# Kernel optimization log

Hardware: AMD Instinct MI355X
Metric: run time of the kernel (lower is better)

The kernel has to match this reference:

```python
import jax, jax.numpy as jnp
import numpy as np

DIM = 256
HEADS = 8
HEAD_DIM = DIM // HEADS
B = 8
HH, WW = 32, 32
N = HH * WW
TABLE = (2 * HH - 1) * (2 * WW - 1)  # 3969
CPB_HID = 512


def _l2norm(t, eps=1e-12):
    # matches torch F.normalize(dim=-1): x / max(||x||, eps)
    n = jnp.sqrt(jnp.sum(t * t, axis=-1, keepdims=True))
    return t / jnp.maximum(n, eps)


def setup_inputs() -> dict:
    key = jax.random.key(0)
    ks = jax.random.split(key, 12)
    x = jax.random.normal(ks[0], (B, N, DIM), dtype=jnp.float32)
    relative_pos_index = jax.random.randint(ks[1], (N, N), 0, TABLE)
    relative_coords_table = jax.random.normal(ks[2], (TABLE, 2), dtype=jnp.float32)
    s = 0.02
    qkv_w = jax.random.normal(ks[3], (3 * DIM, DIM), dtype=jnp.float32) * s
    qkv_b = jnp.zeros((3 * DIM,), dtype=jnp.float32)
    query_embedding = jax.random.normal(ks[4], (HEADS, 1, HEAD_DIM), dtype=jnp.float32) * s
    # temperature init: log(exp(1/0.24) - 1) so softplus(temperature) = 1/0.24
    temperature = jnp.full((HEADS, 1, 1), float(np.log(np.expm1(1.0 / 0.24))), dtype=jnp.float32)
    proj_w = jax.random.normal(ks[5], (DIM, DIM), dtype=jnp.float32) * s
    proj_b = jnp.zeros((DIM,), dtype=jnp.float32)
    cpb_fc1_w = jax.random.normal(ks[6], (CPB_HID, 2), dtype=jnp.float32) * s
    cpb_fc1_b = jnp.zeros((CPB_HID,), dtype=jnp.float32)
    cpb_fc2_w = jax.random.normal(ks[7], (HEADS, CPB_HID), dtype=jnp.float32) * s
    cpb_fc2_b = jnp.zeros((HEADS,), dtype=jnp.float32)
    return dict(x=x, H=HH, W=WW, relative_pos_index=relative_pos_index,
                relative_coords_table=relative_coords_table,
                qkv_w=qkv_w, qkv_b=qkv_b, query_embedding=query_embedding,
                temperature=temperature, proj_w=proj_w, proj_b=proj_b,
                cpb_fc1_w=cpb_fc1_w, cpb_fc1_b=cpb_fc1_b,
                cpb_fc2_w=cpb_fc2_w, cpb_fc2_b=cpb_fc2_b)


def reference(x, H, W, relative_pos_index, relative_coords_table,
              qkv_w, qkv_b, query_embedding, temperature,
              proj_w, proj_b, cpb_fc1_w, cpb_fc1_b, cpb_fc2_w, cpb_fc2_b):
    Bc, Nc, C = x.shape
    seq_length_scale = jnp.asarray(np.log(HH * WW), dtype=x.dtype)  # from init input_resolution
    # qkv projection -> [B, heads, N, head_dim] each
    qkv = (x @ qkv_w.T + qkv_b).reshape(Bc, Nc, 3 * HEADS, HEAD_DIM).transpose(0, 2, 1, 3)
    q, k, v = qkv[:, :HEADS], qkv[:, HEADS:2 * HEADS], qkv[:, 2 * HEADS:]
    # CPB relative position bias: small MLP over coord table, then NxN gather
    h = jax.nn.relu(relative_coords_table @ cpb_fc1_w.T + cpb_fc1_b)  # [T, 512]
    table = (h @ cpb_fc2_w.T + cpb_fc2_b).T                           # [heads, T]
    rel_bias = table[:, relative_pos_index.reshape(-1)].reshape(HEADS, Nc, Nc)
    # cosine attention with learned temperature
    qn = _l2norm(q) + query_embedding[None]                           # [B, heads, N, hd]
    scale = jax.nn.softplus(temperature) * seq_length_scale           # [heads, 1, 1]
    attn = jnp.einsum('bhnd,bhmd->bhnm', qn * scale[None], _l2norm(k)) + rel_bias[None]
    attn = jax.nn.softmax(attn, axis=-1)
    out = jnp.einsum('bhnm,bhmd->bhnd', attn, v).transpose(0, 2, 1, 3).reshape(Bc, Nc, C)
    return out @ proj_w.T + proj_b
```

## Files before the change

kernel.cpp:

```cpp
#include <hip/hip_runtime.h>
#include <hip/hip_bf16.h>
#include <cstddef>
#include <cstdint>

typedef float v4f __attribute__((ext_vector_type(4)));
typedef short v8s __attribute__((ext_vector_type(8)));
typedef _Float16 v8h __attribute__((ext_vector_type(8)));

__device__ __forceinline__ uint32_t fbits(float x){ uint32_t u; __builtin_memcpy(&u,&x,4); return u; }
__device__ __forceinline__ float ffrom(uint32_t u){ float f; __builtin_memcpy(&f,&u,4); return f; }
__device__ __forceinline__ short bf_rh(float x){ return (short)((fbits(x)+0x8000u)>>16); }
__device__ __forceinline__ uint32_t pack_bf_rh(float a, float b){
    uint32_t ua = fbits(a)+0x8000u, ub = fbits(b)+0x8000u;
#if __has_builtin(__builtin_amdgcn_perm)
    return __builtin_amdgcn_perm(ub, ua, 0x07060302u);
#else
    return (ua>>16) | (ub & 0xFFFF0000u);
#endif
}
__device__ __forceinline__ short f2h(float x){ _Float16 h = (_Float16)x; short s; __builtin_memcpy(&s,&h,2); return s; }
#if __has_builtin(__builtin_amdgcn_exp2f)
#define EXP2(x) __builtin_amdgcn_exp2f(x)
#else
#define EXP2(x) exp2f(x)
#endif

__device__ __forceinline__ void gld16(const void* g, void* l) {
    __builtin_amdgcn_global_load_lds(
        (const __attribute__((address_space(1))) unsigned int*)g,
        (__attribute__((address_space(3))) unsigned int*)l, 16, 0, 0);
}
#define MFMA(a,b,c)  __builtin_amdgcn_mfma_f32_16x16x32_bf16((a),(b),(c),0,0,0)
#define MFMAH(a,b,c) __builtin_amdgcn_mfma_f32_16x16x32_f16((a),(b),(c),0,0,0)

#define LOG2E 1.4426950408889634f

__global__ __launch_bounds__(256)
void prep_kernel(const float* __restrict__ x,  short* __restrict__ xh,
                 const float* __restrict__ wq, short* __restrict__ wqh,
                 const float* __restrict__ wp, short* __restrict__ wph,
                 const float* __restrict__ rct,
                 const float* __restrict__ fc1w, const float* __restrict__ fc1b,
                 const float* __restrict__ fc2w, const float* __restrict__ fc2b,
                 float* __restrict__ table)
{
    __shared__ float s1[1024];
    __shared__ float sb[512];
    __shared__ float s2[4096];
    int bid = blockIdx.x;
    int tid = threadIdx.x;
    if (bid < 1152) {
        const float* src; short* dh; int base8;
        if (bid < 1024)      { src = x;  dh = xh;  base8 = bid * 256; }
        else if (bid < 1120) { src = wq; dh = wqh; base8 = (bid-1024) * 256; }
        else                 { src = wp; dh = wph; base8 = (bid-1120) * 256; }
        int e0 = (base8 + tid) * 8;
        int m  = e0 >> 8;
        int k  = e0 & 255;
        int kt = k >> 6, c = (k >> 3) & 7;
        float4 f0 = *(const float4*)(src + e0);
        float4 f1 = *(const float4*)(src + e0 + 4);
        float v[8] = {f0.x,f0.y,f0.z,f0.w,f1.x,f1.y,f1.z,f1.w};
        v8s hi;
        #pragma unroll
        for (int j = 0; j < 8; ++j) hi[j] = f2h(v[j]);
        int dst = m*256 + kt*64 + ((c ^ (m & 7)) << 3);
        *(v8s*)&dh[dst] = hi;
    } else {
        int cbid = bid - 1152;
        for (int i = tid; i < 1024; i += 256) s1[i] = fc1w[i];
        for (int i = tid; i < 512;  i += 256) sb[i] = fc1b[i];
        for (int i = tid; i < 4096; i += 256) s2[i] = fc2w[i];
        __syncthreads();
        int rl = tid >> 2, jp = tid & 3;
        bool ok = rl < 63;
        int r = cbid * 63 + rl;
        float c0 = ok ? rct[2*r]   : 0.f;
        float c1 = ok ? rct[2*r+1] : 0.f;
        float a[8] = {0,0,0,0,0,0,0,0};
        int j0 = jp * 128;
        #pragma unroll 4
        for (int j = j0; j < j0 + 128; ++j) {
            float hv = fmaxf(c0*s1[2*j] + c1*s1[2*j+1] + sb[j], 0.0f);
            #pragma unroll
            for (int hh = 0; hh < 8; ++hh) a[hh] += hv * s2[hh*512 + j];
        }
        #pragma unroll
        for (int hh = 0; hh < 8; ++hh) {
            a[hh] += __shfl_xor(a[hh], 1);
            a[hh] += __shfl_xor(a[hh], 2);
        }
        if (ok && jp == 0) {
            #pragma unroll
            for (int hh = 0; hh < 8; ++hh) table[hh*3969 + r] = a[hh] + fc2b[hh];
        }
    }
}

__global__ __launch_bounds__(256)
void qkv_bias_kernel(const short* __restrict__ xh, const short* __restrict__ wqh,
                     const float* __restrict__ qkvb,
                     short* __restrict__ qh, short* __restrict__ kh,
                     short* __restrict__ vt,
                     const float* __restrict__ qe, const float* __restrict__ temp,
                     const float* __restrict__ tblf, const int* __restrict__ rpi,
                     short* __restrict__ biasM)
{
    __shared__ __align__(16) char smem[49152];
    int bid  = blockIdx.x;
    int tid  = threadIdx.x;
    int w    = tid >> 6;
    int lane = tid & 63;
    int t    = lane & 15;
    int quad = lane >> 4;

    if (bid < 768) {
        short* A0 = (short*)smem;
        short* A1 = A0 + 128*64;
        short* W0 = A1 + 128*64;
        short* W1 = W0 + 64*64;
        int n0 = (bid % 12) * 64, m0 = (bid / 12) * 128;
        int Mw = (w >> 1) * 64, Nw = (w & 1) * 32;

        v4f acc[4][2];
        #pragma unroll
        for (int mt = 0; mt < 4; ++mt)
            #pragma unroll
            for (int nt = 0; nt < 2; ++nt) acc[mt][nt] = (v4f){0,0,0,0};

        int lr8 = lane >> 3, lc8 = lane & 7;
        #pragma unroll 1
        for (int kt2 = 0; kt2 < 2; ++kt2) {
            __syncthreads();
            #pragma unroll
            for (int half = 0; half < 2; ++half) {
                int kt = kt2*2 + half;
                short* Ad = half ? A1 : A0;
                short* Wd = half ? W1 : W0;
                #pragma unroll
                for (int i = 0; i < 4; ++i) {
                    size_t grow = (size_t)(m0 + w*32 + i*8 + lr8) * 256 + kt*64 + lc8*8;
                    gld16(xh + grow, Ad + (w*32 + i*8) * 64);
                }
                #pragma unroll
                for (int i = 0; i < 2; ++i) {
                    size_t grow = (size_t)(n0 + w*16 + i*8 + lr8) * 256 + kt*64 + lc8*8;
                    gld16(wqh + grow, Wd + (w*16 + i*8) * 64);
                }
            }
            __syncthreads();
            #pragma unroll
            for (int half = 0; half < 2; ++half) {
                const short* As = half ? A1 : A0;
                const short* Ws = half ? W1 : W0;
                #pragma unroll
                for (int kk = 0; kk < 2; ++kk) {
                    int cp = ((kk*4 + quad) ^ (t & 7)) << 3;
                    v8h bh8[2];
                    #pragma unroll
                    for (int nt = 0; nt < 2; ++nt)
                        bh8[nt] = *(const v8h*)&Ws[(Nw + nt*16 + t)*64 + cp];
                    #pragma unroll
                    for (int mt = 0; mt < 4; ++mt) {
                        v8h ah = *(const v8h*)&As[(Mw + mt*16 + t)*64 + cp];
                        #pragma unroll
                        for (int nt = 0; nt < 2; ++nt)
                            acc[mt][nt] = MFMAH(ah, bh8[nt], acc[mt][nt]);
                    }
                }
            }
        }

        #pragma unroll
        for (int nt = 0; nt < 2; ++nt) {
            float bv = qkvb[n0 + Nw + nt*16 + t];
            #pragma unroll
            for (int mt = 0; mt < 4; ++mt)
                #pragma unroll
                for (int r = 0; r < 4; ++r) acc[mt][nt][r] += bv;
        }

        int which = n0 >> 8;
        if (which < 2) {
            int head = ((n0 + Nw) >> 5) & 7;
            float scale = 0.f;
            if (which == 0)
                scale = log1pf(__expf(temp[head])) * 10.0f;
            #pragma unroll
            for (int mt = 0; mt < 4; ++mt)
                #pragma unroll
                for (int r = 0; r < 4; ++r) {
                    float a0 = acc[mt][0][r], a1 = acc[mt][1][r];
                    float s = a0*a0 + a1*a1;
                    s += __shfl_xor(s, 1); s += __shfl_xor(s, 2);
                    s += __shfl_xor(s, 4); s += __shfl_xor(s, 8);
                    float inv = 1.0f / fmaxf(sqrtf(s), 1e-12f);
                    int m = m0 + Mw + mt*16 + quad*4 + r;
                    int b = m >> 10, nrow = m & 1023;
                    if (which == 0) {
                        size_t rowoff = (((size_t)b*8 + head)*1024 + nrow) * 32;
                        #pragma unroll
                        for (int nt = 0; nt < 2; ++nt) {
                            int d = nt*16 + t;
                            float val = (acc[mt][nt][r] * inv + qe[head*32 + d]) * scale;
                            qh[rowoff + d] = f2h(val);
                        }
                    } else {
                        int kk = nrow & 63;
                        int p  = (kk & 3)*16 + (kk >> 2);
                        int prow = (nrow & ~63) | p;
                        int swk = (kk >> 3) & 3;
                        size_t rowoff = (((size_t)b*8 + head)*1024 + prow) * 32;
                        #pragma unroll
                        for (int nt = 0; nt < 2; ++nt) {
                            int d = nt*16 + t;
                            int dpos = (((d >> 3) ^ swk) << 3) | (d & 7);
                            kh[rowoff + dpos] = f2h(acc[mt][nt][r] * inv);
                        }
                    }
                }
        } else {
            __syncthreads();
            short* VT = (short*)smem;
            #pragma unroll
            for (int mt = 0; mt < 4; ++mt)
                #pragma unroll
                for (int nt = 0; nt < 2; ++nt) {
                    int cl = Nw + nt*16 + t;
                    #pragma unroll
                    for (int r = 0; r < 4; ++r) {
                        int rl = Mw + mt*16 + quad*4 + r;
                        VT[cl*136 + rl] = bf_rh(acc[mt][nt][r]);
                    }
                }
            __syncthreads();
            int b = m0 >> 10;
            int keybase = m0 & 1023;
            int headbase = ((n0 - 512) >> 5) & 7;
            int cl = tid >> 2;
            int dim = cl & 31;
            int hd  = headbase + (cl >> 5);
            size_t obase = (((size_t)b*8 + hd)*32 + dim) * 1024 + keybase;
            #pragma unroll
            for (int p = 0; p < 4; ++p) {
                int ci  = (tid & 3) * 4 + p;
                int ktl = ci >> 3, c = ci & 7;
                v8s val = *(const v8s*)&VT[cl*136 + ktl*64 + c*8];
                *(v8s*)&vt[obase + ktl*64 + ((c ^ (dim & 7)) << 3)] = val;
            }
        }
    } else {
        float* tb = (float*)smem;
        int b2  = bid - 768;
        int h   = b2 & 7;
        int q16 = b2 >> 3;
        for (int i = tid; i < 3969; i += 256) tb[i] = tblf[h*3969 + i] * LOG2E;
        __syncthreads();
        int row0 = q16*16 + quad*4;
        #pragma unroll 1
        for (int kk = 0; kk < 4; ++kk) {
            int kt = w*4 + kk;
            #pragma unroll
            for (int g = 0; g < 4; ++g) {
                float o[4];
                #pragma unroll
                for (int r = 0; r < 4; ++r)
                    o[r] = tb[rpi[(size_t)(row0 + r)*1024 + kt*64 + 4*t + g]];
                uint2 pk;
                pk.x = pack_bf_rh(o[0], o[1]);
                pk.y = pack_bf_rh(o[2], o[3]);
                size_t base = ((((size_t)(h*64 + q16)*16 + kt)*4 + g)*64 + lane)*4;
                *(uint2*)(biasM + base) = pk;
            }
        }
    }
}

__global__ __launch_bounds__(512)
void attn_mfma(const short* __restrict__ qh, const short* __restrict__ kh,
               const short* __restrict__ vt,  const short* __restrict__ biasM,
               short* __restrict__ yh)
{
    __shared__ __align__(16) short Kh_s[2][2048];
    __shared__ __align__(16) short Vt_s[2][2048];
    __shared__ __align__(16) short Ps[8][16][68];

    int bh  = blockIdx.x & 63;
    int qt  = blockIdx.x >> 6;
    int h   = bh & 7;
    int b   = bh >> 3;
    int tid = threadIdx.x;
    int w    = tid >> 6;
    int lane = tid & 63;
    int t    = lane & 15;
    int quad = lane >> 4;

    size_t qoff = ((size_t)bh*1024 + qt*128 + w*16 + t) * 32 + quad*8;
    v8h qf = *(const v8h*)(qh + qoff);

    v4f Oacc[2] = {{0,0,0,0},{0,0,0,0}};
    float lsum[4] = {0,0,0,0};

    size_t kgbase = (size_t)bh * 32768;
    const short* bmb = biasM + ((size_t)(h*64 + qt*8 + w) * 16) * 1024 + lane*4;
    int qrow0 = qt*128 + w*16 + quad*4;
    int swzS = (quad ^ ((t >> 1) & 3)) << 3;
    int lr8 = lane >> 3, lc8 = lane & 7;

    if (w < 4)
        gld16(kh + kgbase + w*512 + lane*8, &Kh_s[0][w*512]);
    else
        gld16(vt + kgbase + (size_t)((w-4)*8 + lr8)*1024 + lc8*8, &Vt_s[0][(w-4)*512]);
    uint2 curb[4];
    #pragma unroll
    for (int g = 0; g < 4; ++g) curb[g] = *(const uint2*)(bmb + g*256);

    #pragma unroll 1
    for (int kt = 0; kt < 16; ++kt) {
        int cur = kt & 1;
        __syncthreads();
        uint2 nxtb[4];
        if (kt < 15) {
            int nkt = kt + 1, nb = cur ^ 1;
            if (w < 4)
                gld16(kh + kgbase + (size_t)nkt*2048 + w*512 + lane*8, &Kh_s[nb][w*512]);
            else
                gld16(vt + kgbase + (size_t)((w-4)*8 + lr8)*1024 + nkt*64 + lc8*8,
                      &Vt_s[nb][(w-4)*512]);
            const short* bp = bmb + (size_t)nkt*1024;
            #pragma unroll
            for (int g = 0; g < 4; ++g) nxtb[g] = *(const uint2*)(bp + g*256);
        }

        v4f S[4];
        #pragma unroll
        for (int g = 0; g < 4; ++g) {
            v8h kb = *(const v8h*)&Kh_s[cur][(g*16 + t)*32 + swzS];
            v4f c;
            c[0] = ffrom(curb[g].x << 16);
            c[1] = ffrom(curb[g].x & 0xFFFF0000u);
            c[2] = ffrom(curb[g].y << 16);
            c[3] = ffrom(curb[g].y & 0xFFFF0000u);
            S[g] = MFMAH(qf, kb, c);
        }

        #pragma unroll
        for (int r = 0; r < 4; ++r) {
            float p0 = EXP2(S[0][r]);
            float p1 = EXP2(S[1][r]);
            float p2 = EXP2(S[2][r]);
            float p3 = EXP2(S[3][r]);
            lsum[r] += (p0 + p1) + (p2 + p3);
            uint2 pk;
            pk.x = pack_bf_rh(p0, p1);
            pk.y = pack_bf_rh(p2, p3);
            *(uint2*)&Ps[w][quad*4 + r][t*4] = pk;
        }

        #pragma unroll
        for (int ks = 0; ks < 2; ++ks) {
            v8s pf = *(const v8s*)&Ps[w][t][ks*32 + quad*8];
            int vsw = ((ks*4 + quad) ^ (t & 7)) << 3;
            #pragma unroll
            for (int g = 0; g < 2; ++g) {
                v8s vf = *(const v8s*)&Vt_s[cur][(g*16 + t)*64 + vsw];
                Oacc[g] = MFMA(pf, vf, Oacc[g]);
            }
        }
        #pragma unroll
        for (int g = 0; g < 4; ++g) curb[g] = nxtb[g];
    }

    #pragma unroll
    for (int r = 0; r < 4; ++r) {
        float l = lsum[r];
        l += __shfl_xor(l, 1); l += __shfl_xor(l, 2);
        l += __shfl_xor(l, 4); l += __shfl_xor(l, 8);
        float inv = 1.0f / l;
        int qrow = qrow0 + r;
        int m = b*1024 + qrow;
        size_t mbase = (size_t)m * 256;
        int mk = m & 7;
        #pragma unroll
        for (int g = 0; g < 2; ++g) {
            float o = Oacc[g][r] * inv;
            int c = h*4 + g*2 + (t >> 3);
            int chp = ((c ^ mk) << 3) | (t & 7);
            yh[mbase + chp] = f2h(o);
        }
    }
}

__global__ __launch_bounds__(256)
void gemm_proj(const short* __restrict__ Ah_g, const short* __restrict__ Wh_g,
               const float* __restrict__ bias, float* __restrict__ C, int N)
{
    __shared__ __align__(16) short As[2][4096];
    __shared__ __align__(16) short Ws[2][4096];

    int tid  = threadIdx.x;
    int w    = tid >> 6;
    int lane = tid & 63;
    int t    = lane & 15;
    int quad = lane >> 4;
    int m0 = blockIdx.y * 64, n0 = blockIdx.x * 64;
    int Mw = (w >> 1) * 32, Nw = (w & 1) * 32;

    v4f acc[2][2];
    #pragma unroll
    for (int mt = 0; mt < 2; ++mt)
        #pragma unroll
        for (int nt = 0; nt < 2; ++nt) acc[mt][nt] = (v4f){0,0,0,0};

    int lr8 = lane >> 3, lc8 = lane & 7;
    #pragma unroll 1
    for (int kt2 = 0; kt2 < 2; ++kt2) {
        __syncthreads();
        #pragma unroll
        for (int half = 0; half < 2; ++half) {
            int kt = kt2*2 + half;
            #pragma unroll
            for (int i = 0; i < 2; ++i) {
                size_t grow = (size_t)(m0 + w*16 + i*8 + lr8) * 256 + kt*64 + lc8*8;
                gld16(Ah_g + grow, &As[half][(w*16 + i*8) * 64]);
            }
            #pragma unroll
            for (int i = 0; i < 2; ++i) {
                size_t grow = (size_t)(n0 + w*16 + i*8 + lr8) * 256 + kt*64 + lc8*8;
                gld16(Wh_g + grow, &Ws[half][(w*16 + i*8) * 64]);
            }
        }
        __syncthreads();
        #pragma unroll
        for (int half = 0; half < 2; ++half) {
            #pragma unroll
            for (int kk = 0; kk < 2; ++kk) {
                int cp = ((kk*4 + quad) ^ (t & 7)) << 3;
                v8h bh8[2];
                #pragma unroll
                for (int nt = 0; nt < 2; ++nt)
                    bh8[nt] = *(const v8h*)&Ws[half][(Nw + nt*16 + t)*64 + cp];
                #pragma unroll
                for (int mt = 0; mt < 2; ++mt) {
                    v8h ah = *(const v8h*)&As[half][(Mw + mt*16 + t)*64 + cp];
                    #pragma unroll
                    for (int nt = 0; nt < 2; ++nt)
                        acc[mt][nt] = MFMAH(ah, bh8[nt], acc[mt][nt]);
                }
            }
        }
    }

    #pragma unroll
    for (int nt = 0; nt < 2; ++nt) {
        float bv = bias[n0 + Nw + nt*16 + t];
        #pragma unroll
        for (int mt = 0; mt < 2; ++mt)
            #pragma unroll
            for (int r = 0; r < 4; ++r) acc[mt][nt][r] += bv;
    }
    #pragma unroll
    for (int mt = 0; mt < 2; ++mt)
        #pragma unroll
        for (int r = 0; r < 4; ++r) {
            int m = m0 + Mw + mt*16 + quad*4 + r;
            #pragma unroll
            for (int nt = 0; nt < 2; ++nt)
                C[(size_t)m * N + n0 + Nw + nt*16 + t] = acc[mt][nt][r];
        }
}

extern "C" void kernel_launch(void* const* d_in, const int* in_sizes, int n_in,
                              void* d_out, int out_size, void* d_ws, size_t ws_size,
                              hipStream_t stream)
{
    const float* x     = (const float*)d_in[0];
    const int*   rpi   = (const int*)d_in[3];
    const float* rct   = (const float*)d_in[4];
    const float* qkvw  = (const float*)d_in[5];
    const float* qkvb  = (const float*)d_in[6];
    const float* qe    = (const float*)d_in[7];
    const float* temp  = (const float*)d_in[8];
    const float* projw = (const float*)d_in[9];
    const float* projb = (const float*)d_in[10];
    const float* fc1w  = (const float*)d_in[11];
    const float* fc1b  = (const float*)d_in[12];
    const float* fc2w  = (const float*)d_in[13];
    const float* fc2b  = (const float*)d_in[14];

    char* p = (char*)d_ws;
    float* tblf  = (float*)p;  p += 131072;
    short* xh    = (short*)p;  p += 4194304;
    short* wqh   = (short*)p;  p += 393216;
    short* wph   = (short*)p;  p += 131072;
    short* qh    = (short*)p;  p += 4194304;
    short* kh    = (short*)p;  p += 4194304;
    short* vt    = (short*)p;  p += 4194304;
    short* biasM = (short*)p;  p += 16777216;
    float* out   = (float*)d_out;

    prep_kernel<<<1215, 256, 0, stream>>>(x, xh, qkvw, wqh, projw, wph,
                                          rct, fc1w, fc1b, fc2w, fc2b, tblf);

    qkv_bias_kernel<<<1280, 256, 0, stream>>>(xh, wqh, qkvb, qh, kh, vt,
                                              qe, temp, tblf, rpi, biasM);

    attn_mfma<<<512, 512, 0, stream>>>(qh, kh, vt, biasM, xh);

    dim3 g2(256/64, 8192/64);
    gemm_proj<<<g2, 256, 0, stream>>>(xh, wph, projb, out, 256);
}
```

Before: 149.4 us.

## Fuse four pipeline stages into one cooperative persistent kernel with grid syncs

Replaces the four separate launches (prep, qkv+bias, attention, projection) with a single cooperative persistent kernel that loops over work units per stage and separates stages with grid.sync, falling back to the old launches if cooperative launch fails. The goal is to remove inter-kernel launch gaps and tail effects. In exchange, the attention stage now runs with 256 threads per block instead of 512 and no longer double-buffers across different block counts. The grid is capped at 512 blocks, and each grid barrier adds its own cost.

```diff
diff --git a/kernel.cpp b/kernel.cpp
--- a/kernel.cpp
+++ b/kernel.cpp
@@ -1,7 +1,10 @@
 #include <hip/hip_runtime.h>
+#include <hip/hip_cooperative_groups.h>
 #include <hip/hip_bf16.h>
 #include <cstddef>
 #include <cstdint>
+
+namespace cg = cooperative_groups;
 
 typedef float v4f __attribute__((ext_vector_type(4)));
 typedef short v8s __attribute__((ext_vector_type(8)));
@@ -207,8 +210,8 @@
                         }
                     } else {
                         int kk = nrow & 63;
-                        int p  = (kk & 3)*16 + (kk >> 2);
-                        int prow = (nrow & ~63) | p;
+                        int pp = (kk & 3)*16 + (kk >> 2);
+                        int prow = (nrow & ~63) | pp;
                         int swk = (kk >> 3) & 3;
                         size_t rowoff = (((size_t)b*8 + head)*1024 + prow) * 32;
                         #pragma unroll
@@ -242,8 +245,8 @@
             int hd  = headbase + (cl >> 5);
             size_t obase = (((size_t)b*8 + hd)*32 + dim) * 1024 + keybase;
             #pragma unroll
-            for (int p = 0; p < 4; ++p) {
-                int ci  = (tid & 3) * 4 + p;
+            for (int pz = 0; pz < 4; ++pz) {
+                int ci  = (tid & 3) * 4 + pz;
                 int ktl = ci >> 3, c = ci & 7;
                 v8s val = *(const v8s*)&VT[cl*136 + ktl*64 + c*8];
                 *(v8s*)&vt[obase + ktl*64 + ((c ^ (dim & 7)) << 3)] = val;
@@ -252,9 +255,9 @@
     } else {
         float* tb = (float*)smem;
         int b2  = bid - 768;
-        int h   = b2 & 7;
+        int h2  = b2 & 7;
         int q16 = b2 >> 3;
-        for (int i = tid; i < 3969; i += 256) tb[i] = tblf[h*3969 + i] * LOG2E;
+        for (int i = tid; i < 3969; i += 256) tb[i] = tblf[h2*3969 + i] * LOG2E;
         __syncthreads();
         int row0 = q16*16 + quad*4;
         #pragma unroll 1
@@ -269,7 +272,7 @@
                 uint2 pk;
                 pk.x = pack_bf_rh(o[0], o[1]);
                 pk.y = pack_bf_rh(o[2], o[3]);
-                size_t base = ((((size_t)(h*64 + q16)*16 + kt)*4 + g)*64 + lane)*4;
+                size_t base = ((((size_t)(h2*64 + q16)*16 + kt)*4 + g)*64 + lane)*4;
                 *(uint2*)(biasM + base) = pk;
             }
         }
@@ -468,6 +471,439 @@
             for (int nt = 0; nt < 2; ++nt)
                 C[(size_t)m * N + n0 + Nw + nt*16 + t] = acc[mt][nt][r];
         }
+}
+
+__global__ __launch_bounds__(256, 2)
+void mega(const float* __restrict__ x,    const float* __restrict__ wq,
+          const float* __restrict__ wp,   const float* __restrict__ rct,
+          const float* __restrict__ fc1w, const float* __restrict__ fc1b,
+          const float* __restrict__ fc2w, const float* __restrict__ fc2b,
+          const float* __restrict__ qkvb, const float* __restrict__ qe,
+          const float* __restrict__ temp, const int*   __restrict__ rpi,
+          const float* __restrict__ projb, float* __restrict__ out,
+          short* __restrict__ xh,  short* __restrict__ wqh,
+          short* __restrict__ wph, float* __restrict__ tblf,
+          short* __restrict__ qh,  short* __restrict__ kh,
+          short* __restrict__ vt,  short* __restrict__ biasM)
+{
+    cg::grid_group grid = cg::this_grid();
+    __shared__ __align__(16) char smem[49152];
+    int bid  = blockIdx.x;
+    int G    = gridDim.x;
+    int tid  = threadIdx.x;
+    int w    = tid >> 6;
+    int lane = tid & 63;
+    int t    = lane & 15;
+    int quad = lane >> 4;
+    int lr8  = lane >> 3, lc8 = lane & 7;
+
+    for (int u = bid; u < 1215; u += G) {
+        if (u < 1152) {
+            const float* src; short* dh; int base8;
+            if (u < 1024)      { src = x;  dh = xh;  base8 = u * 256; }
+            else if (u < 1120) { src = wq; dh = wqh; base8 = (u-1024) * 256; }
+            else               { src = wp; dh = wph; base8 = (u-1120) * 256; }
+            int e0 = (base8 + tid) * 8;
+            int m  = e0 >> 8;
+            int k  = e0 & 255;
+            int kt = k >> 6, c = (k >> 3) & 7;
+            float4 f0 = *(const float4*)(src + e0);
+            float4 f1 = *(const float4*)(src + e0 + 4);
+            float v[8] = {f0.x,f0.y,f0.z,f0.w,f1.x,f1.y,f1.z,f1.w};
+            v8s hi;
+            #pragma unroll
+            for (int j = 0; j < 8; ++j) hi[j] = f2h(v[j]);
+            int dst = m*256 + kt*64 + ((c ^ (m & 7)) << 3);
+            *(v8s*)&dh[dst] = hi;
+        } else {
+            __syncthreads();
+            float* s1 = (float*)smem;
+            float* sb = s1 + 1024;
+            float* s2 = sb + 512;
+            int cbid = u - 1152;
+            for (int i = tid; i < 1024; i += 256) s1[i] = fc1w[i];
+            for (int i = tid; i < 512;  i += 256) sb[i] = fc1b[i];
+            for (int i = tid; i < 4096; i += 256) s2[i] = fc2w[i];
+            __syncthreads();
+            int rl = tid >> 2, jp = tid & 3;
+            bool ok = rl < 63;
+            int r = cbid * 63 + rl;
+            float c0 = ok ? rct[2*r]   : 0.f;
+            float c1 = ok ? rct[2*r+1] : 0.f;
+            float a[8] = {0,0,0,0,0,0,0,0};
+            int j0 = jp * 128;
+            #pragma unroll 4
+            for (int j = j0; j < j0 + 128; ++j) {
+                float hv = fmaxf(c0*s1[2*j] + c1*s1[2*j+1] + sb[j], 0.0f);
+                #pragma unroll
+                for (int hh = 0; hh < 8; ++hh) a[hh] += hv * s2[hh*512 + j];
+            }
+            #pragma unroll
+            for (int hh = 0; hh < 8; ++hh) {
+                a[hh] += __shfl_xor(a[hh], 1);
+                a[hh] += __shfl_xor(a[hh], 2);
+            }
+            if (ok && jp == 0) {
+                #pragma unroll
+                for (int hh = 0; hh < 8; ++hh) tblf[hh*3969 + r] = a[hh] + fc2b[hh];
+            }
+        }
+    }
+
+    grid.sync();
+
+    for (int u = bid; u < 1280; u += G) {
+        __syncthreads();
+        if (u < 768) {
+            short* A0 = (short*)smem;
+            short* A1 = A0 + 128*64;
+            short* W0 = A1 + 128*64;
+            short* W1 = W0 + 64*64;
+            int n0 = (u % 12) * 64, m0 = (u / 12) * 128;
+            int Mw = (w >> 1) * 64, Nw = (w & 1) * 32;
+
+            v4f acc[4][2];
+            #pragma unroll
+            for (int mt = 0; mt < 4; ++mt)
+                #pragma unroll
+                for (int nt = 0; nt < 2; ++nt) acc[mt][nt] = (v4f){0,0,0,0};
+
+            #pragma unroll 1
+            for (int kt2 = 0; kt2 < 2; ++kt2) {
+                __syncthreads();
+                #pragma unroll
+                for (int half = 0; half < 2; ++half) {
+                    int kt = kt2*2 + half;
+                    short* Ad = half ? A1 : A0;
+                    short* Wd = half ? W1 : W0;
+                    #pragma unroll
+                    for (int i = 0; i < 4; ++i) {
+                        size_t grow = (size_t)(m0 + w*32 + i*8 + lr8) * 256 + kt*64 + lc8*8;
+                        gld16(xh + grow, Ad + (w*32 + i*8) * 64);
+                    }
+                    #pragma unroll
+                    for (int i = 0; i < 2; ++i) {
+                        size_t grow = (size_t)(n0 + w*16 + i*8 + lr8) * 256 + kt*64 + lc8*8;
+                        gld16(wqh + grow, Wd + (w*16 + i*8) * 64);
+                    }
+                }
+                __syncthreads();
+                #pragma unroll
+                for (int half = 0; half < 2; ++half) {
+                    const short* As = half ? A1 : A0;
+                    const short* Ws = half ? W1 : W0;
+                    #pragma unroll
+                    for (int kk = 0; kk < 2; ++kk) {
+                        int cp = ((kk*4 + quad) ^ (t & 7)) << 3;
+                        v8h bh8[2];
+                        #pragma unroll
+                        for (int nt = 0; nt < 2; ++nt)
+                            bh8[nt] = *(const v8h*)&Ws[(Nw + nt*16 + t)*64 + cp];
+                        #pragma unroll
+                        for (int mt = 0; mt < 4; ++mt) {
+                            v8h ah = *(const v8h*)&As[(Mw + mt*16 + t)*64 + cp];
+                            #pragma unroll
+                            for (int nt = 0; nt < 2; ++nt)
+                                acc[mt][nt] = MFMAH(ah, bh8[nt], acc[mt][nt]);
+                        }
+                    }
+                }
+            }
+
+            #pragma unroll
+            for (int nt = 0; nt < 2; ++nt) {
+                float bv = qkvb[n0 + Nw + nt*16 + t];
+                #pragma unroll
+                for (int mt = 0; mt < 4; ++mt)
+                    #pragma unroll
+                    for (int r = 0; r < 4; ++r) acc[mt][nt][r] += bv;
+            }
+
+            int which = n0 >> 8;
+            if (which < 2) {
+                int head = ((n0 + Nw) >> 5) & 7;
+                float scale = 0.f;
+                if (which == 0)
+                    scale = log1pf(__expf(temp[head])) * 10.0f;
+                #pragma unroll
+                for (int mt = 0; mt < 4; ++mt)
+                    #pragma unroll
+                    for (int r = 0; r < 4; ++r) {
+                        float a0 = acc[mt][0][r], a1 = acc[mt][1][r];
+                        float s = a0*a0 + a1*a1;
+                        s += __shfl_xor(s, 1); s += __shfl_xor(s, 2);
+                        s += __shfl_xor(s, 4); s += __shfl_xor(s, 8);
+                        float inv = 1.0f / fmaxf(sqrtf(s), 1e-12f);
+                        int m = m0 + Mw + mt*16 + quad*4 + r;
+                        int b = m >> 10, nrow = m & 1023;
+                        if (which == 0) {
+                            size_t rowoff = (((size_t)b*8 + head)*1024 + nrow) * 32;
+                            #pragma unroll
+                            for (int nt = 0; nt < 2; ++nt) {
+                                int d = nt*16 + t;
+                                float val = (acc[mt][nt][r] * inv + qe[head*32 + d]) * scale;
+                                qh[rowoff + d] = f2h(val);
+                            }
+                        } else {
+                            int kk = nrow & 63;
+                            int pp = (kk & 3)*16 + (kk >> 2);
+                            int prow = (nrow & ~63) | pp;
+                            int swk = (kk >> 3) & 3;
+                            size_t rowoff = (((size_t)b*8 + head)*1024 + prow) * 32;
+                            #pragma unroll
+                            for (int nt = 0; nt < 2; ++nt) {
+                                int d = nt*16 + t;
+                                int dpos = (((d >> 3) ^ swk) << 3) | (d & 7);
+                                kh[rowoff + dpos] = f2h(acc[mt][nt][r] * inv);
+                            }
+                        }
+                    }
+            } else {
+                __syncthreads();
+                short* VT = (short*)smem;
+                #pragma unroll
+                for (int mt = 0; mt < 4; ++mt)
+                    #pragma unroll
+                    for (int nt = 0; nt < 2; ++nt) {
+                        int cl = Nw + nt*16 + t;
+                        #pragma unroll
+                        for (int r = 0; r < 4; ++r) {
+                            int rl = Mw + mt*16 + quad*4 + r;
+                            VT[cl*136 + rl] = bf_rh(acc[mt][nt][r]);
+                        }
+                    }
+                __syncthreads();
+                int b = m0 >> 10;
+                int keybase = m0 & 1023;
+                int headbase = ((n0 - 512) >> 5) & 7;
+                int cl = tid >> 2;
+                int dim = cl & 31;
+                int hd  = headbase + (cl >> 5);
+                size_t obase = (((size_t)b*8 + hd)*32 + dim) * 1024 + keybase;
+                #pragma unroll
+                for (int pz = 0; pz < 4; ++pz) {
+                    int ci  = (tid & 3) * 4 + pz;
+                    int ktl = ci >> 3, c = ci & 7;
+                    v8s val = *(const v8s*)&VT[cl*136 + ktl*64 + c*8];
+                    *(v8s*)&vt[obase + ktl*64 + ((c ^ (dim & 7)) << 3)] = val;
+                }
+            }
+        } else {
+            float* tb = (float*)smem;
+            int b2  = u - 768;
+            int h2  = b2 & 7;
+            int q16 = b2 >> 3;
+            for (int i = tid; i < 3969; i += 256) tb[i] = tblf[h2*3969 + i] * LOG2E;
+            __syncthreads();
+            int row0 = q16*16 + quad*4;
+            #pragma unroll 1
+            for (int kk = 0; kk < 4; ++kk) {
+                int kt = w*4 + kk;
+                #pragma unroll
+                for (int g = 0; g < 4; ++g) {
+                    float o[4];
+                    #pragma unroll
+                    for (int r = 0; r < 4; ++r)
+                        o[r] = tb[rpi[(size_t)(row0 + r)*1024 + kt*64 + 4*t + g]];
+                    uint2 pk;
+                    pk.x = pack_bf_rh(o[0], o[1]);
+                    pk.y = pack_bf_rh(o[2], o[3]);
+                    size_t base = ((((size_t)(h2*64 + q16)*16 + kt)*4 + g)*64 + lane)*4;
+                    *(uint2*)(biasM + base) = pk;
+                }
+            }
+        }
+    }
+
+    grid.sync();
+
+    for (int u = bid; u < 1024; u += G) {
+        int bh  = u & 63;
+        int qt2 = u >> 6;
+        int h   = bh & 7;
+        int b   = bh >> 3;
+        short* Kh  = (short*)smem;
+        short* Vts = Kh + 4096;
+        short* Psb = Vts + 4096;
+
+        size_t qoff = ((size_t)bh*1024 + qt2*64 + w*16 + t) * 32 + quad*8;
+        v8h qf = *(const v8h*)(qh + qoff);
+
+        v4f Oacc[2] = {{0,0,0,0},{0,0,0,0}};
+        float lsum[4] = {0,0,0,0};
+
+        size_t kgbase = (size_t)bh * 32768;
+        const short* bmb = biasM + ((size_t)(h*64 + qt2*4 + w) * 16) * 1024 + lane*4;
+        int qrow0 = qt2*64 + w*16 + quad*4;
+        int swzS = (quad ^ ((t >> 1) & 3)) << 3;
+
+        __syncthreads();
+        if (w < 2) {
+            gld16(kh + kgbase + (w*2+0)*512 + lane*8, &Kh[(w*2+0)*512]);
+            gld16(kh + kgbase + (w*2+1)*512 + lane*8, &Kh[(w*2+1)*512]);
+        } else {
+            int v0 = w - 2;
+            gld16(vt + kgbase + (size_t)(v0*16 + lr8)*1024 + lc8*8,     &Vts[(v0*2+0)*512]);
+            gld16(vt + kgbase + (size_t)(v0*16 + 8 + lr8)*1024 + lc8*8, &Vts[(v0*2+1)*512]);
+        }
+        uint2 curb[4];
+        #pragma unroll
+        for (int g = 0; g < 4; ++g) curb[g] = *(const uint2*)(bmb + g*256);
+
+        #pragma unroll 1
+        for (int kt = 0; kt < 16; ++kt) {
+            int cur = kt & 1;
+            __syncthreads();
+            uint2 nxtb[4];
+            if (kt < 15) {
+                int nkt = kt + 1, nb = cur ^ 1;
+                if (w < 2) {
+                    gld16(kh + kgbase + (size_t)nkt*2048 + (w*2+0)*512 + lane*8,
+                          &Kh[nb*2048 + (w*2+0)*512]);
+                    gld16(kh + kgbase + (size_t)nkt*2048 + (w*2+1)*512 + lane*8,
+                          &Kh[nb*2048 + (w*2+1)*512]);
+                } else {
+                    int v0 = w - 2;
+                    gld16(vt + kgbase + (size_t)(v0*16 + lr8)*1024 + nkt*64 + lc8*8,
+                          &Vts[nb*2048 + (v0*2+0)*512]);
+                    gld16(vt + kgbase + (size_t)(v0*16 + 8 + lr8)*1024 + nkt*64 + lc8*8,
+                          &Vts[nb*2048 + (v0*2+1)*512]);
+                }
+                const short* bp = bmb + (size_t)nkt*1024;
+                #pragma unroll
+                for (int g = 0; g < 4; ++g) nxtb[g] = *(const uint2*)(bp + g*256);
+            }
+
+            v4f S[4];
+            #pragma unroll
+            for (int g = 0; g < 4; ++g) {
+                v8h kb = *(const v8h*)&Kh[cur*2048 + (g*16 + t)*32 + swzS];
+                v4f c;
+                c[0] = ffrom(curb[g].x << 16);
+                c[1] = ffrom(curb[g].x & 0xFFFF0000u);
+                c[2] = ffrom(curb[g].y << 16);
+                c[3] = ffrom(curb[g].y & 0xFFFF0000u);
+                S[g] = MFMAH(qf, kb, c);
+            }
+
+            #pragma unroll
+            for (int r = 0; r < 4; ++r) {
+                float p0 = EXP2(S[0][r]);
+                float p1 = EXP2(S[1][r]);
+                float p2 = EXP2(S[2][r]);
+                float p3 = EXP2(S[3][r]);
+                lsum[r] += (p0 + p1) + (p2 + p3);
+                uint2 pk;
+                pk.x = pack_bf_rh(p0, p1);
+                pk.y = pack_bf_rh(p2, p3);
+                *(uint2*)&Psb[(w*16 + quad*4 + r)*68 + t*4] = pk;
+            }
+
+            #pragma unroll
+            for (int ks = 0; ks < 2; ++ks) {
+                v8s pf = *(const v8s*)&Psb[(w*16 + t)*68 + ks*32 + quad*8];
+                int vsw = ((ks*4 + quad) ^ (t & 7)) << 3;
+                #pragma unroll
+                for (int g = 0; g < 2; ++g) {
+                    v8s vf = *(const v8s*)&Vts[cur*2048 + (g*16 + t)*64 + vsw];
+                    Oacc[g] = MFMA(pf, vf, Oacc[g]);
+                }
+            }
+            #pragma unroll
+            for (int g = 0; g < 4; ++g) curb[g] = nxtb[g];
+        }
+
+        #pragma unroll
+        for (int r = 0; r < 4; ++r) {
+            float l = lsum[r];
+            l += __shfl_xor(l, 1); l += __shfl_xor(l, 2);
+            l += __shfl_xor(l, 4); l += __shfl_xor(l, 8);
+            float inv = 1.0f / l;
+            int qrow = qrow0 + r;
+            int m = b*1024 + qrow;
+            size_t mbase = (size_t)m * 256;
+            int mk = m & 7;
+            #pragma unroll
+            for (int g = 0; g < 2; ++g) {
+                float o = Oacc[g][r] * inv;
+                int c = h*4 + g*2 + (t >> 3);
+                int chp = ((c ^ mk) << 3) | (t & 7);
+                xh[mbase + chp] = f2h(o);
+            }
+        }
+    }
+
+    grid.sync();
+
+    for (int u = bid; u < 512; u += G) {
+        int m0 = (u >> 2) * 64, n0 = (u & 3) * 64;
+        short* As = (short*)smem;
+        short* Ws = As + 8192;
+
+        int Mw = (w >> 1) * 32, Nw = (w & 1) * 32;
+
+        v4f acc[2][2];
+        #pragma unroll
+        for (int mt = 0; mt < 2; ++mt)
+            #pragma unroll
+            for (int nt = 0; nt < 2; ++nt) acc[mt][nt] = (v4f){0,0,0,0};
+
+        #pragma unroll 1
+        for (int kt2 = 0; kt2 < 2; ++kt2) {
+            __syncthreads();
+            #pragma unroll
+            for (int half = 0; half < 2; ++half) {
+                int kt = kt2*2 + half;
+                #pragma unroll
+                for (int i = 0; i < 2; ++i) {
+                    size_t grow = (size_t)(m0 + w*16 + i*8 + lr8) * 256 + kt*64 + lc8*8;
+                    gld16(xh + grow, As + half*4096 + (w*16 + i*8) * 64);
+                }
+                #pragma unroll
+                for (int i = 0; i < 2; ++i) {
+                    size_t grow = (size_t)(n0 + w*16 + i*8 + lr8) * 256 + kt*64 + lc8*8;
+                    gld16(wph + grow, Ws + half*4096 + (w*16 + i*8) * 64);
+                }
+            }
+            __syncthreads();
+            #pragma unroll
+            for (int half = 0; half < 2; ++half) {
+                #pragma unroll
+                for (int kk = 0; kk < 2; ++kk) {
+                    int cp = ((kk*4 + quad) ^ (t & 7)) << 3;
+                    v8h bh8[2];
+                    #pragma unroll
+                    for (int nt = 0; nt < 2; ++nt)
+                        bh8[nt] = *(const v8h*)&Ws[half*4096 + (Nw + nt*16 + t)*64 + cp];
+                    #pragma unroll
+                    for (int mt = 0; mt < 2; ++mt) {
+                        v8h ah = *(const v8h*)&As[half*4096 + (Mw + mt*16 + t)*64 + cp];
+                        #pragma unroll
+                        for (int nt = 0; nt < 2; ++nt)
+                            acc[mt][nt] = MFMAH(ah, bh8[nt], acc[mt][nt]);
+                    }
+                }
+            }
+        }
+
+        #pragma unroll
+        for (int nt = 0; nt < 2; ++nt) {
+            float bv = projb[n0 + Nw + nt*16 + t];
+            #pragma unroll
+            for (int mt = 0; mt < 2; ++mt)
+                #pragma unroll
+                for (int r = 0; r < 4; ++r) acc[mt][nt][r] += bv;
+        }
+        #pragma unroll
+        for (int mt = 0; mt < 2; ++mt)
+            #pragma unroll
+            for (int r = 0; r < 4; ++r) {
+                int m = m0 + Mw + mt*16 + quad*4 + r;
+                #pragma unroll
+                for (int nt = 0; nt < 2; ++nt)
+                    out[(size_t)m * 256 + n0 + Nw + nt*16 + t] = acc[mt][nt][r];
+            }
+    }
 }
 
 extern "C" void kernel_launch(void* const* d_in, const int* in_sizes, int n_in,
@@ -499,14 +935,43 @@
     short* biasM = (short*)p;  p += 16777216;
     float* out   = (float*)d_out;
 
-    prep_kernel<<<1215, 256, 0, stream>>>(x, xh, qkvw, wqh, projw, wph,
-                                          rct, fc1w, fc1b, fc2w, fc2b, tblf);
-
-    qkv_bias_kernel<<<1280, 256, 0, stream>>>(xh, wqh, qkvb, qh, kh, vt,
-                                              qe, temp, tblf, rpi, biasM);
-
-    attn_mfma<<<512, 512, 0, stream>>>(qh, kh, vt, biasM, xh);
-
-    dim3 g2(256/64, 8192/64);
-    gemm_proj<<<g2, 256, 0, stream>>>(xh, wph, projb, out, 256);
+    static int coop_grid = -1;
+    if (coop_grid == -1) {
+        int nb = 0, cus = 0, dev = 0;
+        if (hipOccupancyMaxActiveBlocksPerMultiprocessor(
+                &nb, (const void*)mega, 256, 0) != hipSuccess) nb = 0;
+        hipGetDevice(&dev);
+        hipDeviceProp_t prop;
+        if (hipGetDeviceProperties(&prop, dev) == hipSuccess)
+            cus = prop.multiProcessorCount;
+        long cap = (long)nb * (long)cus;
+        coop_grid = (cap >= 512) ? 512 : (cap >= 64 ? (int)cap : 0);
+    }
+
+    bool launched = false;
+    if (coop_grid > 0) {
+        void* args[] = {
+            (void*)&x,    (void*)&qkvw, (void*)&projw, (void*)&rct,
+            (void*)&fc1w, (void*)&fc1b, (void*)&fc2w,  (void*)&fc2b,
+            (void*)&qkvb, (void*)&qe,   (void*)&temp,  (void*)&rpi,
+            (void*)&projb,(void*)&out,
+            (void*)&xh,   (void*)&wqh,  (void*)&wph,   (void*)&tblf,
+            (void*)&qh,   (void*)&kh,   (void*)&vt,    (void*)&biasM
+        };
+        hipError_t e = hipLaunchCooperativeKernel((const void*)mega,
+                                                  dim3(coop_grid), dim3(256),
+                                                  args, 0, stream);
+        if (e == hipSuccess) launched = true;
+        else coop_grid = 0;
+    }
+
+    if (!launched) {
+        prep_kernel<<<1215, 256, 0, stream>>>(x, xh, qkvw, wqh, projw, wph,
+                                              rct, fc1w, fc1b, fc2w, fc2b, tblf);
+        qkv_bias_kernel<<<1280, 256, 0, stream>>>(xh, wqh, qkvb, qh, kh, vt,
+                                                  qe, temp, tblf, rpi, biasM);
+        attn_mfma<<<512, 512, 0, stream>>>(qh, kh, vt, biasM, xh);
+        dim3 g2(256/64, 8192/64);
+        gemm_proj<<<g2, 256, 0, stream>>>(xh, wph, projb, out, 256);
+    }
 }
```

Result: slower. 309.6 us (+107.2%).

## Replace materialized bias matrix with packed indices and LDS table gather, fuse prep

Applied to the files above, without the earlier changes.

The separate prep kernel is merged into the QKV kernel. The QKV GEMM now reads fp32 x and weights directly and converts them to fp16 while staging into LDS, so the fp16 copies of x and qkv_w are no longer written to and read back from global memory. The dense per-head bf16 bias matrix (16 MB) is no longer built. A 2 MB array of packed 16-bit relative-position indices, shared by all heads, is built instead, and the attention kernel looks up the bias from a per-head fp32 table held in LDS. This cuts global memory traffic and removes one launch. In exchange, every score tile now does extra LDS gathers that may hit bank conflicts, and attention uses more LDS per block.

```diff
diff --git a/kernel.cpp b/kernel.cpp
--- a/kernel.cpp
+++ b/kernel.cpp
@@ -36,75 +36,15 @@
 #define LOG2E 1.4426950408889634f
 
 __global__ __launch_bounds__(256)
-void prep_kernel(const float* __restrict__ x,  short* __restrict__ xh,
-                 const float* __restrict__ wq, short* __restrict__ wqh,
-                 const float* __restrict__ wp, short* __restrict__ wph,
-                 const float* __restrict__ rct,
-                 const float* __restrict__ fc1w, const float* __restrict__ fc1b,
-                 const float* __restrict__ fc2w, const float* __restrict__ fc2b,
-                 float* __restrict__ table)
-{
-    __shared__ float s1[1024];
-    __shared__ float sb[512];
-    __shared__ float s2[4096];
-    int bid = blockIdx.x;
-    int tid = threadIdx.x;
-    if (bid < 1152) {
-        const float* src; short* dh; int base8;
-        if (bid < 1024)      { src = x;  dh = xh;  base8 = bid * 256; }
-        else if (bid < 1120) { src = wq; dh = wqh; base8 = (bid-1024) * 256; }
-        else                 { src = wp; dh = wph; base8 = (bid-1120) * 256; }
-        int e0 = (base8 + tid) * 8;
-        int m  = e0 >> 8;
-        int k  = e0 & 255;
-        int kt = k >> 6, c = (k >> 3) & 7;
-        float4 f0 = *(const float4*)(src + e0);
-        float4 f1 = *(const float4*)(src + e0 + 4);
-        float v[8] = {f0.x,f0.y,f0.z,f0.w,f1.x,f1.y,f1.z,f1.w};
-        v8s hi;
-        #pragma unroll
-        for (int j = 0; j < 8; ++j) hi[j] = f2h(v[j]);
-        int dst = m*256 + kt*64 + ((c ^ (m & 7)) << 3);
-        *(v8s*)&dh[dst] = hi;
-    } else {
-        int cbid = bid - 1152;
-        for (int i = tid; i < 1024; i += 256) s1[i] = fc1w[i];
-        for (int i = tid; i < 512;  i += 256) sb[i] = fc1b[i];
-        for (int i = tid; i < 4096; i += 256) s2[i] = fc2w[i];
-        __syncthreads();
-        int rl = tid >> 2, jp = tid & 3;
-        bool ok = rl < 63;
-        int r = cbid * 63 + rl;
-        float c0 = ok ? rct[2*r]   : 0.f;
-        float c1 = ok ? rct[2*r+1] : 0.f;
-        float a[8] = {0,0,0,0,0,0,0,0};
-        int j0 = jp * 128;
-        #pragma unroll 4
-        for (int j = j0; j < j0 + 128; ++j) {
-            float hv = fmaxf(c0*s1[2*j] + c1*s1[2*j+1] + sb[j], 0.0f);
-            #pragma unroll
-            for (int hh = 0; hh < 8; ++hh) a[hh] += hv * s2[hh*512 + j];
-        }
-        #pragma unroll
-        for (int hh = 0; hh < 8; ++hh) {
-            a[hh] += __shfl_xor(a[hh], 1);
-            a[hh] += __shfl_xor(a[hh], 2);
-        }
-        if (ok && jp == 0) {
-            #pragma unroll
-            for (int hh = 0; hh < 8; ++hh) table[hh*3969 + r] = a[hh] + fc2b[hh];
-        }
-    }
-}
-
-__global__ __launch_bounds__(256)
-void qkv_bias_kernel(const short* __restrict__ xh, const short* __restrict__ wqh,
-                     const float* __restrict__ qkvb,
-                     short* __restrict__ qh, short* __restrict__ kh,
-                     short* __restrict__ vt,
-                     const float* __restrict__ qe, const float* __restrict__ temp,
-                     const float* __restrict__ tblf, const int* __restrict__ rpi,
-                     short* __restrict__ biasM)
+void fused_qkv(const float* __restrict__ x,   const float* __restrict__ wq,
+               const float* __restrict__ wp,  const float* __restrict__ rct,
+               const float* __restrict__ fc1w, const float* __restrict__ fc1b,
+               const float* __restrict__ fc2w, const float* __restrict__ fc2b,
+               const float* __restrict__ qkvb, const float* __restrict__ qe,
+               const float* __restrict__ temp, const int* __restrict__ rpi,
+               short* __restrict__ qh, short* __restrict__ kh,
+               short* __restrict__ vt, float* __restrict__ tblf,
+               short* __restrict__ wph, unsigned long long* __restrict__ bi)
 {
     __shared__ __align__(16) char smem[49152];
     int bid  = blockIdx.x;
@@ -113,13 +53,75 @@
     int lane = tid & 63;
     int t    = lane & 15;
     int quad = lane >> 4;
-
-    if (bid < 768) {
+    int lr8  = lane >> 3, lc8 = lane & 7;
+
+    if (bid < 63) {
+        float* s1 = (float*)smem;
+        float* sb = s1 + 1024;
+        float* s2 = sb + 512;
+        for (int i = tid; i < 1024; i += 256) s1[i] = fc1w[i];
+        for (int i = tid; i < 512;  i += 256) sb[i] = fc1b[i];
+        for (int i = tid; i < 4096; i += 256) s2[i] = fc2w[i];
+        __syncthreads();
+        int rl = tid >> 2, jp = tid & 3;
+        bool ok = rl < 63;
+        int r = bid * 63 + rl;
+        float c0 = ok ? rct[2*r]   : 0.f;
+        float c1 = ok ? rct[2*r+1] : 0.f;
+        float a[8] = {0,0,0,0,0,0,0,0};
+        int j0 = jp * 128;
+        #pragma unroll 4
+        for (int j = j0; j < j0 + 128; ++j) {
+            float hv = fmaxf(c0*s1[2*j] + c1*s1[2*j+1] + sb[j], 0.0f);
+            #pragma unroll
+            for (int hh = 0; hh < 8; ++hh) a[hh] += hv * s2[hh*512 + j];
+        }
+        #pragma unroll
+        for (int hh = 0; hh < 8; ++hh) {
+            a[hh] += __shfl_xor(a[hh], 1);
+            a[hh] += __shfl_xor(a[hh], 2);
+        }
+        if (ok && jp == 0) {
+            #pragma unroll
+            for (int hh = 0; hh < 8; ++hh)
+                tblf[hh*3969 + r] = (a[hh] + fc2b[hh]) * LOG2E;
+        }
+    } else if (bid < 95) {
+        int base8 = (bid - 63) * 256;
+        int e0 = (base8 + tid) * 8;
+        int m  = e0 >> 8;
+        int k  = e0 & 255;
+        int kt = k >> 6, c = (k >> 3) & 7;
+        float4 f0 = *(const float4*)(wp + e0);
+        float4 f1 = *(const float4*)(wp + e0 + 4);
+        float v[8] = {f0.x,f0.y,f0.z,f0.w,f1.x,f1.y,f1.z,f1.w};
+        v8s hi;
+        #pragma unroll
+        for (int j = 0; j < 8; ++j) hi[j] = f2h(v[j]);
+        int dst = m*256 + kt*64 + ((c ^ (m & 7)) << 3);
+        *(v8s*)&wph[dst] = hi;
+    } else if (bid < 159) {
+        int q16 = bid - 95;
+        int grp = tid >> 6;
+        #pragma unroll 1
+        for (int c = 0; c < 16; ++c) {
+            int combo = grp*16 + c;
+            int kt = combo >> 2, g = combo & 3;
+            unsigned long long pk = 0;
+            #pragma unroll
+            for (int r = 0; r < 4; ++r) {
+                int idx = rpi[(size_t)(q16*16 + quad*4 + r)*1024 + kt*64 + 4*t + g];
+                pk |= (unsigned long long)(idx & 0xFFFF) << (16*r);
+            }
+            bi[((size_t)(q16*16 + kt)*4 + g)*64 + lane] = pk;
+        }
+    } else {
         short* A0 = (short*)smem;
         short* A1 = A0 + 128*64;
         short* W0 = A1 + 128*64;
         short* W1 = W0 + 64*64;
-        int n0 = (bid % 12) * 64, m0 = (bid / 12) * 128;
+        int g2 = bid - 159;
+        int n0 = (g2 % 12) * 64, m0 = (g2 / 12) * 128;
         int Mw = (w >> 1) * 64, Nw = (w & 1) * 32;
 
         v4f acc[4][2];
@@ -128,7 +130,6 @@
             #pragma unroll
             for (int nt = 0; nt < 2; ++nt) acc[mt][nt] = (v4f){0,0,0,0};
 
-        int lr8 = lane >> 3, lc8 = lane & 7;
         #pragma unroll 1
         for (int kt2 = 0; kt2 < 2; ++kt2) {
             __syncthreads();
@@ -139,13 +140,29 @@
                 short* Wd = half ? W1 : W0;
                 #pragma unroll
                 for (int i = 0; i < 4; ++i) {
-                    size_t grow = (size_t)(m0 + w*32 + i*8 + lr8) * 256 + kt*64 + lc8*8;
-                    gld16(xh + grow, Ad + (w*32 + i*8) * 64);
+                    int rr = w*32 + i*8 + lr8;
+                    const float* s = x + (size_t)(m0 + rr)*256 + kt*64 + lc8*8;
+                    float4 f0 = *(const float4*)s;
+                    float4 f1 = *(const float4*)(s + 4);
+                    v8h hv;
+                    hv[0]=(_Float16)f0.x; hv[1]=(_Float16)f0.y;
+                    hv[2]=(_Float16)f0.z; hv[3]=(_Float16)f0.w;
+                    hv[4]=(_Float16)f1.x; hv[5]=(_Float16)f1.y;
+                    hv[6]=(_Float16)f1.z; hv[7]=(_Float16)f1.w;
+                    *(v8h*)&Ad[rr*64 + ((lc8 ^ lr8) << 3)] = hv;
                 }
                 #pragma unroll
                 for (int i = 0; i < 2; ++i) {
-                    size_t grow = (size_t)(n0 + w*16 + i*8 + lr8) * 256 + kt*64 + lc8*8;
-                    gld16(wqh + grow, Wd + (w*16 + i*8) * 64);
+                    int rr = w*16 + i*8 + lr8;
+                    const float* s = wq + (size_t)(n0 + rr)*256 + kt*64 + lc8*8;
+                    float4 f0 = *(const float4*)s;
+                    float4 f1 = *(const float4*)(s + 4);
+                    v8h hv;
+                    hv[0]=(_Float16)f0.x; hv[1]=(_Float16)f0.y;
+                    hv[2]=(_Float16)f0.z; hv[3]=(_Float16)f0.w;
+                    hv[4]=(_Float16)f1.x; hv[5]=(_Float16)f1.y;
+                    hv[6]=(_Float16)f1.z; hv[7]=(_Float16)f1.w;
+                    *(v8h*)&Wd[rr*64 + ((lc8 ^ lr8) << 3)] = hv;
                 }
             }
             __syncthreads();
@@ -207,8 +224,8 @@
                         }
                     } else {
                         int kk = nrow & 63;
-                        int p  = (kk & 3)*16 + (kk >> 2);
-                        int prow = (nrow & ~63) | p;
+                        int pp = (kk & 3)*16 + (kk >> 2);
+                        int prow = (nrow & ~63) | pp;
                         int swk = (kk >> 3) & 3;
                         size_t rowoff = (((size_t)b*8 + head)*1024 + prow) * 32;
                         #pragma unroll
@@ -242,48 +259,27 @@
             int hd  = headbase + (cl >> 5);
             size_t obase = (((size_t)b*8 + hd)*32 + dim) * 1024 + keybase;
             #pragma unroll
-            for (int p = 0; p < 4; ++p) {
-                int ci  = (tid & 3) * 4 + p;
+            for (int pz = 0; pz < 4; ++pz) {
+                int ci  = (tid & 3) * 4 + pz;
                 int ktl = ci >> 3, c = ci & 7;
                 v8s val = *(const v8s*)&VT[cl*136 + ktl*64 + c*8];
                 *(v8s*)&vt[obase + ktl*64 + ((c ^ (dim & 7)) << 3)] = val;
             }
         }
-    } else {
-        float* tb = (float*)smem;
-        int b2  = bid - 768;
-        int h   = b2 & 7;
-        int q16 = b2 >> 3;
-        for (int i = tid; i < 3969; i += 256) tb[i] = tblf[h*3969 + i] * LOG2E;
-        __syncthreads();
-        int row0 = q16*16 + quad*4;
-        #pragma unroll 1
-        for (int kk = 0; kk < 4; ++kk) {
-            int kt = w*4 + kk;
-            #pragma unroll
-            for (int g = 0; g < 4; ++g) {
-                float o[4];
-                #pragma unroll
-                for (int r = 0; r < 4; ++r)
-                    o[r] = tb[rpi[(size_t)(row0 + r)*1024 + kt*64 + 4*t + g]];
-                uint2 pk;
-                pk.x = pack_bf_rh(o[0], o[1]);
-                pk.y = pack_bf_rh(o[2], o[3]);
-                size_t base = ((((size_t)(h*64 + q16)*16 + kt)*4 + g)*64 + lane)*4;
-                *(uint2*)(biasM + base) = pk;
-            }
-        }
     }
 }
 
 __global__ __launch_bounds__(512)
 void attn_mfma(const short* __restrict__ qh, const short* __restrict__ kh,
-               const short* __restrict__ vt,  const short* __restrict__ biasM,
+               const short* __restrict__ vt,
+               const unsigned long long* __restrict__ bi,
+               const float* __restrict__ tblf,
                short* __restrict__ yh)
 {
     __shared__ __align__(16) short Kh_s[2][2048];
     __shared__ __align__(16) short Vt_s[2][2048];
     __shared__ __align__(16) short Ps[8][16][68];
+    __shared__ float tb[3972];
 
     int bh  = blockIdx.x & 63;
     int qt  = blockIdx.x >> 6;
@@ -295,6 +291,8 @@
     int t    = lane & 15;
     int quad = lane >> 4;
 
+    for (int i = tid; i < 3969; i += 512) tb[i] = tblf[h*3969 + i];
+
     size_t qoff = ((size_t)bh*1024 + qt*128 + w*16 + t) * 32 + quad*8;
     v8h qf = *(const v8h*)(qh + qoff);
 
@@ -302,7 +300,7 @@
     float lsum[4] = {0,0,0,0};
 
     size_t kgbase = (size_t)bh * 32768;
-    const short* bmb = biasM + ((size_t)(h*64 + qt*8 + w) * 16) * 1024 + lane*4;
+    const unsigned long long* bmb = bi + (size_t)(qt*8 + w)*4096 + lane;
     int qrow0 = qt*128 + w*16 + quad*4;
     int swzS = (quad ^ ((t >> 1) & 3)) << 3;
     int lr8 = lane >> 3, lc8 = lane & 7;
@@ -311,15 +309,15 @@
         gld16(kh + kgbase + w*512 + lane*8, &Kh_s[0][w*512]);
     else
         gld16(vt + kgbase + (size_t)((w-4)*8 + lr8)*1024 + lc8*8, &Vt_s[0][(w-4)*512]);
-    uint2 curb[4];
+    unsigned long long curb[4];
     #pragma unroll
-    for (int g = 0; g < 4; ++g) curb[g] = *(const uint2*)(bmb + g*256);
+    for (int g = 0; g < 4; ++g) curb[g] = bmb[g*64];
 
     #pragma unroll 1
     for (int kt = 0; kt < 16; ++kt) {
         int cur = kt & 1;
         __syncthreads();
-        uint2 nxtb[4];
+        unsigned long long nxtb[4];
         if (kt < 15) {
             int nkt = kt + 1, nb = cur ^ 1;
             if (w < 4)
@@ -327,20 +325,20 @@
             else
                 gld16(vt + kgbase + (size_t)((w-4)*8 + lr8)*1024 + nkt*64 + lc8*8,
                       &Vt_s[nb][(w-4)*512]);
-            const short* bp = bmb + (size_t)nkt*1024;
-            #pragma unroll
-            for (int g = 0; g < 4; ++g) nxtb[g] = *(const uint2*)(bp + g*256);
+            #pragma unroll
+            for (int g = 0; g < 4; ++g) nxtb[g] = bmb[nkt*256 + g*64];
         }
 
         v4f S[4];
         #pragma unroll
         for (int g = 0; g < 4; ++g) {
             v8h kb = *(const v8h*)&Kh_s[cur][(g*16 + t)*32 + swzS];
+            unsigned long long cb = curb[g];
             v4f c;
-            c[0] = ffrom(curb[g].x << 16);
-            c[1] = ffrom(curb[g].x & 0xFFFF0000u);
-            c[2] = ffrom(curb[g].y << 16);
-            c[3] = ffrom(curb[g].y & 0xFFFF0000u);
+            c[0] = tb[(uint32_t)cb & 0xFFFFu];
+            c[1] = tb[(uint32_t)(cb >> 16) & 0xFFFFu];
+            c[2] = tb[(uint32_t)(cb >> 32) & 0xFFFFu];
+            c[3] = tb[(uint32_t)(cb >> 48)];
             S[g] = MFMAH(qf, kb, c);
         }
 
@@ -490,23 +488,21 @@
 
     char* p = (char*)d_ws;
     float* tblf  = (float*)p;  p += 131072;
-    short* xh    = (short*)p;  p += 4194304;
-    short* wqh   = (short*)p;  p += 393216;
+    short* y     = (short*)p;  p += 4194304;
     short* wph   = (short*)p;  p += 131072;
     short* qh    = (short*)p;  p += 4194304;
     short* kh    = (short*)p;  p += 4194304;
     short* vt    = (short*)p;  p += 4194304;
-    short* biasM = (short*)p;  p += 16777216;
+    unsigned long long* bi = (unsigned long long*)p; p += 2097152;
     float* out   = (float*)d_out;
 
-    prep_kernel<<<1215, 256, 0, stream>>>(x, xh, qkvw, wqh, projw, wph,
-                                          rct, fc1w, fc1b, fc2w, fc2b, tblf);
-
-    qkv_bias_kernel<<<1280, 256, 0, stream>>>(xh, wqh, qkvb, qh, kh, vt,
-                                              qe, temp, tblf, rpi, biasM);
-
-    attn_mfma<<<512, 512, 0, stream>>>(qh, kh, vt, biasM, xh);
+    fused_qkv<<<927, 256, 0, stream>>>(x, qkvw, projw, rct,
+                                       fc1w, fc1b, fc2w, fc2b,
+                                       qkvb, qe, temp, rpi,
+                                       qh, kh, vt, tblf, wph, bi);
+
+    attn_mfma<<<512, 512, 0, stream>>>(qh, kh, vt, bi, tblf, y);
 
     dim3 g2(256/64, 8192/64);
-    gemm_proj<<<g2, 256, 0, stream>>>(xh, wph, projb, out, 256);
+    gemm_proj<<<g2, 256, 0, stream>>>(y, wph, projb, out, 256);
 }
```

Measured after the change: 148.4 us. About the same (-0.7%).
